# Performance work log

Measured on AMD Instinct MI355X. Metric: run time of the kernel, lower is better.

Reference implementation:

```python
import jax, jax.numpy as jnp
import numpy as np

N = 50000
E = 1600000
D = 128
BN_EPS = 1e-5


def setup_inputs() -> dict:
    key = jax.random.key(0)
    ks = jax.random.split(key, 6)
    feature = jax.random.normal(ks[0], (N, D), dtype=jnp.float32)
    snorm_n = jax.random.uniform(ks[1], (N, 1), dtype=jnp.float32)
    src = jax.random.randint(ks[2], (E,), 0, N, dtype=jnp.int64)
    dst = jax.random.randint(ks[3], (E,), 0, N, dtype=jnp.int64)
    W = jax.random.normal(ks[4], (D, D), dtype=jnp.float32) * (1.0 / np.sqrt(D))
    b = jax.random.normal(ks[5], (D,), dtype=jnp.float32) * 0.01
    gamma = jnp.ones((D,), dtype=jnp.float32)
    beta = jnp.zeros((D,), dtype=jnp.float32)
    return {"feature": feature, "snorm_n": snorm_n, "src": src, "dst": dst,
            "W": W, "b": b, "gamma": gamma, "beta": beta}


def reference(feature, snorm_n, src, dst, W, b, gamma, beta):
    # --- copy_src + mean reduce (DGL update_all) ---
    msg = feature[src]                                    # [E, D] gather
    agg = jax.ops.segment_sum(msg, dst, num_segments=N)   # [N, D] scatter-add
    deg = jax.ops.segment_sum(jnp.ones((src.shape[0],), feature.dtype), dst,
                              num_segments=N)             # [N]
    has_msg = deg > 0
    mean = agg / jnp.maximum(deg, 1.0)[:, None]
    # nodes with no incoming edges keep their original 'h' (DGL semantics)
    h = jnp.where(has_msg[:, None], mean, feature)
    # --- apply_nodes: linear ---
    h = h @ W.T + b
    # --- graph norm ---
    h = h * snorm_n
    # --- batch norm (training-mode stats, biased variance, eps=1e-5) ---
    mu = jnp.mean(h, axis=0)
    var = jnp.mean((h - mu) ** 2, axis=0)
    h = (h - mu) / jnp.sqrt(var + BN_EPS) * gamma + beta
    # --- activation + residual (dropout p=0 -> identity) ---
    h = jax.nn.relu(h)
    h = feature + h
    return h
```

## Files before the change

kernel.cpp:

```cpp
#include <hip/hip_runtime.h>

#define D 128
#define BN_EPS 1e-5f
#define ROWS 16
#define CHUNK 8192
#define CAP_SCAN 256
#define HSTRIDE 136
#define P2CAP 12288

typedef unsigned int u32;
typedef unsigned short u16;
typedef __attribute__((ext_vector_type(8))) __bf16 bf16x8;
typedef __attribute__((ext_vector_type(4))) float f32x4;

__device__ inline u32 pk_bf16(float x, float y) {
    u32 ux = __float_as_uint(x), uy = __float_as_uint(y);
    ux = (ux + 0x7fffu + ((ux >> 16) & 1u)) >> 16;
    uy = (uy + 0x7fffu + ((uy >> 16) & 1u)) >> 16;
    return ux | (uy << 16);
}

__global__ __launch_bounds__(256) void prep(const float* __restrict__ feat,
                                            u16* __restrict__ feat16,
                                            const float* __restrict__ W,
                                            u16* __restrict__ Wb,
                                            const int* __restrict__ dst,
                                            int* __restrict__ blkcnt,
                                            int ncast, int nch, int nedges) {
    __shared__ int cnt[256];
    const int b = blockIdx.x;
    if (b < ncast) {
        size_t i = ((size_t)b * 256 + threadIdx.x) * 8;
        float4 f0 = *reinterpret_cast<const float4*>(feat + i);
        float4 f1 = *reinterpret_cast<const float4*>(feat + i + 4);
        uint4 o;
        o.x = pk_bf16(f0.x, f0.y);
        o.y = pk_bf16(f0.z, f0.w);
        o.z = pk_bf16(f1.x, f1.y);
        o.w = pk_bf16(f1.z, f1.w);
        *reinterpret_cast<uint4*>(feat16 + i) = o;
    } else if (b < ncast + 8) {
        int t = (b - ncast) * 256 + threadIdx.x;
        int ct = t >> 8;
        int ks = (t >> 6) & 3;
        int l = t & 63;
        int row_w = 16 * ct + (l & 15);
        int col0 = ks * 32 + (l >> 4) * 8;
        float4 f0 = *reinterpret_cast<const float4*>(W + row_w * D + col0);
        float4 f1 = *reinterpret_cast<const float4*>(W + row_w * D + col0 + 4);
        uint4 o;
        o.x = pk_bf16(f0.x, f0.y);
        o.y = pk_bf16(f0.z, f0.w);
        o.z = pk_bf16(f1.x, f1.y);
        o.w = pk_bf16(f1.z, f1.w);
        *reinterpret_cast<uint4*>(Wb + (size_t)t * 8) = o;
    } else {
        const int c = b - ncast - 8;
        cnt[threadIdx.x] = 0;
        __syncthreads();
        const int e0 = c * CHUNK;
        for (int r = 0; r < CHUNK / 256; ++r) {
            int e = e0 + r * 256 + threadIdx.x;
            if (e < nedges) atomicAdd(&cnt[dst[e] >> 8], 1);
        }
        __syncthreads();
        blkcnt[(size_t)threadIdx.x * nch + c] = cnt[threadIdx.x];
    }
}

__global__ __launch_bounds__(CAP_SCAN) void scanB1(int* __restrict__ blkcnt,
                                                   int* __restrict__ gtot,
                                                   int nch) {
    __shared__ int s[CAP_SCAN];
    const int t = threadIdx.x;
    const size_t row = (size_t)blockIdx.x * nch;
    int v = (t < nch) ? blkcnt[row + t] : 0;
    s[t] = v;
    __syncthreads();
    for (int off = 1; off < CAP_SCAN; off <<= 1) {
        int u = (t >= off) ? s[t - off] : 0;
        __syncthreads();
        s[t] += u;
        __syncthreads();
    }
    if (t < nch) blkcnt[row + t] = s[t] - v;
    if (t == 0) gtot[blockIdx.x] = s[CAP_SCAN - 1];
}

__global__ __launch_bounds__(256) void scanB2(const int* __restrict__ gtot,
                                              int* __restrict__ bucket_base,
                                              int* __restrict__ bucket_cnt) {
    __shared__ int s[256];
    const int t = threadIdx.x;
    int v = gtot[t];
    s[t] = v;
    __syncthreads();
    for (int off = 1; off < 256; off <<= 1) {
        int u = (t >= off) ? s[t - off] : 0;
        __syncthreads();
        s[t] += u;
        __syncthreads();
    }
    bucket_base[t] = s[t] - v;
    bucket_cnt[t] = v;
}

__global__ __launch_bounds__(512) void passB(const int* __restrict__ src,
                                             const int* __restrict__ dst,
                                             const int* __restrict__ blkcnt,
                                             const int* __restrict__ bucket_base,
                                             u32* __restrict__ gpacked,
                                             int nch, int nedges) {
    __shared__ u32 sval[CHUNK];
    __shared__ u16 sbuck[CHUNK];
    __shared__ int cnt[256], lo[256], gbase[256];
    const int t = threadIdx.x;
    const int e0 = blockIdx.x * CHUNK;
    const int m = min(CHUNK, nedges - e0);
    if (t < 256) {
        cnt[t] = 0;
        gbase[t] = blkcnt[(size_t)t * nch + blockIdx.x] + bucket_base[t];
    }
    __syncthreads();
    for (int k = t; k < m; k += 512) atomicAdd(&cnt[dst[e0 + k] >> 8], 1);
    __syncthreads();
    int v = (t < 256) ? cnt[t] : 0;
    if (t < 256) lo[t] = v;
    __syncthreads();
    for (int off = 1; off < 256; off <<= 1) {
        int u = (t >= off && t < 256) ? lo[t - off] : 0;
        __syncthreads();
        if (t < 256) lo[t] += u;
        __syncthreads();
    }
    if (t < 256) { int ex = lo[t] - v; lo[t] = ex; cnt[t] = ex; }
    __syncthreads();
    for (int k = t; k < m; k += 512) {
        int d = dst[e0 + k];
        int b = d >> 8;
        int p = atomicAdd(&cnt[b], 1);
        sval[p] = (u32)src[e0 + k] | ((u32)(d & 255) << 16);
        sbuck[p] = (u16)b;
    }
    __syncthreads();
    for (int i = t; i < m; i += 512) {
        int b = sbuck[i];
        gpacked[gbase[b] + (i - lo[b])] = sval[i];
    }
}

__global__ __launch_bounds__(512) void pass2(const u32* __restrict__ gpacked,
                                             const int* __restrict__ bucket_base,
                                             const int* __restrict__ bucket_cnt,
                                             u16* __restrict__ epos,
                                             int* __restrict__ count,
                                             int* __restrict__ offs,
                                             int nnodes) {
    __shared__ u16 sepos[P2CAP];
    __shared__ int cnt[256], lo[256], cur[256];
    const int t = threadIdx.x;
    const int b = blockIdx.x;
    const int nE = bucket_cnt[b];
    const int base = bucket_base[b];
    if (t < 256) cnt[t] = 0;
    __syncthreads();
    for (int i = t; i < nE; i += 512) atomicAdd(&cnt[gpacked[base + i] >> 16], 1);
    __syncthreads();
    int v = (t < 256) ? cnt[t] : 0;
    if (t < 256) lo[t] = v;
    __syncthreads();
    for (int off = 1; off < 256; off <<= 1) {
        int u = (t >= off && t < 256) ? lo[t - off] : 0;
        __syncthreads();
        if (t < 256) lo[t] += u;
        __syncthreads();
    }
    if (t < 256) {
        int excl = lo[t] - v;
        int n = (b << 8) + t;
        if (n < nnodes) { count[n] = v; offs[n] = base + excl; }
        cur[t] = excl;
    }
    __syncthreads();
    if (nE <= P2CAP) {
        for (int i = t; i < nE; i += 512) {
            u32 p = gpacked[base + i];
            int pos = atomicAdd(&cur[p >> 16], 1);
            sepos[pos] = (u16)(p & 0xffffu);
        }
        __syncthreads();
        for (int i = t; i < nE; i += 512) epos[base + i] = sepos[i];
    } else {
        for (int i = t; i < nE; i += 512) {
            u32 p = gpacked[base + i];
            int pos = atomicAdd(&cur[p >> 16], 1);
            epos[base + pos] = (u16)(p & 0xffffu);
        }
    }
}

__global__ __launch_bounds__(256, 8) void fused_agg_linear(
        const float* __restrict__ feat,
        const u16* __restrict__ feat16,
        const float* __restrict__ snorm,
        const int* __restrict__ offs,
        const int* __restrict__ count,
        const u16* __restrict__ epos,
        const u16* __restrict__ Wb,
        const float* __restrict__ bias,
        float* __restrict__ y,
        float* __restrict__ partial) {
    __shared__ u16 hs16[ROWS][HSTRIDE];
    const int row0 = blockIdx.x * ROWS;
    const int wid = threadIdx.x >> 6;
    const int lane = threadIdx.x & 63;
    const int q = lane >> 4;
    const int ql = lane & 15;

#define LDB(s) (*reinterpret_cast<const uint4*>(feat16 + (size_t)(s) * D + 8 * ql))
#define ADD8(a, u) { \
    a[0] += __uint_as_float((u).x << 16); a[1] += __uint_as_float((u).x & 0xffff0000u); \
    a[2] += __uint_as_float((u).y << 16); a[3] += __uint_as_float((u).y & 0xffff0000u); \
    a[4] += __uint_as_float((u).z << 16); a[5] += __uint_as_float((u).z & 0xffff0000u); \
    a[6] += __uint_as_float((u).w << 16); a[7] += __uint_as_float((u).w & 0xffff0000u); }

    for (int rr = 0; rr < 4; ++rr) {
        const int r = wid * 4 + rr;
        const int n = row0 + r;
        const int dg = count[n];
        const u16* ep = epos + offs[n];
        float a0[8], a1[8];
        #pragma unroll
        for (int k = 0; k < 8; ++k) { a0[k] = 0.0f; a1[k] = 0.0f; }

        int j = 0;
        for (; j + 8 <= dg; j += 8) {
            int s0 = (int)ep[j + q];
            int s1 = (int)ep[j + 4 + q];
            uint4 u0 = LDB(s0);
            uint4 u1 = LDB(s1);
            ADD8(a0, u0);
            ADD8(a1, u1);
        }
        {
            int i0 = j + q, i1 = j + 4 + q;
            if (i0 < dg) { uint4 u0 = LDB((int)ep[i0]); ADD8(a0, u0); }
            if (i1 < dg) { uint4 u1 = LDB((int)ep[i1]); ADD8(a1, u1); }
        }

        float av[8];
        #pragma unroll
        for (int k = 0; k < 8; ++k) {
            float v = a0[k] + a1[k];
            v += __shfl_xor(v, 16, 64);
            v += __shfl_xor(v, 32, 64);
            av[k] = v;
        }
        if (dg > 0) {
            float inv = 1.0f / (float)dg;
            #pragma unroll
            for (int k = 0; k < 8; ++k) av[k] *= inv;
        } else {
            float4 f0 = *reinterpret_cast<const float4*>(feat + (size_t)n * D + 8 * ql);
            float4 f1 = *reinterpret_cast<const float4*>(feat + (size_t)n * D + 8 * ql + 4);
            av[0] = f0.x; av[1] = f0.y; av[2] = f0.z; av[3] = f0.w;
            av[4] = f1.x; av[5] = f1.y; av[6] = f1.z; av[7] = f1.w;
        }
        if (q == 0) {
            uint4 o4;
            o4.x = pk_bf16(av[0], av[1]);
            o4.y = pk_bf16(av[2], av[3]);
            o4.z = pk_bf16(av[4], av[5]);
            o4.w = pk_bf16(av[6], av[7]);
            *reinterpret_cast<uint4*>(&hs16[r][8 * ql]) = o4;
        }
    }
#undef LDB
#undef ADD8
    __syncthreads();

    bf16x8 afrag[4];
    const int arow = lane & 15;
    const int acol0 = (lane >> 4) * 8;
    #pragma unroll
    for (int ks = 0; ks < 4; ++ks)
        afrag[ks] = *reinterpret_cast<const bf16x8*>(&hs16[arow][ks * 32 + acol0]);

    #pragma unroll
    for (int c2 = 0; c2 < 2; ++c2) {
        const int ct = wid * 2 + c2;
        f32x4 acc = {0.f, 0.f, 0.f, 0.f};
        #pragma unroll
        for (int ks = 0; ks < 4; ++ks) {
            bf16x8 bfrag = *reinterpret_cast<const bf16x8*>(
                Wb + ((size_t)(ct * 4 + ks) * 64 + lane) * 8);
            acc = __builtin_amdgcn_mfma_f32_16x16x32_bf16(afrag[ks], bfrag, acc, 0, 0, 0);
        }
        const int col = ct * 16 + (lane & 15);
        const float bb = bias[col];
        float psum = 0.0f, psq = 0.0f;
        #pragma unroll
        for (int i = 0; i < 4; ++i) {
            const int rrow = (lane >> 4) * 4 + i;
            const int n = row0 + rrow;
            float v = (acc[i] + bb) * snorm[n];
            y[(size_t)n * D + col] = v;
            psum += v;
            psq += v * v;
        }
        psum += __shfl_xor(psum, 16, 64);
        psq  += __shfl_xor(psq, 16, 64);
        psum += __shfl_xor(psum, 32, 64);
        psq  += __shfl_xor(psq, 32, 64);
        if (lane < 16) {
            partial[(size_t)blockIdx.x * 256 + col] = psum;
            partial[(size_t)blockIdx.x * 256 + 128 + col] = psq;
        }
    }
}

__global__ __launch_bounds__(256) void bn_reduce(const float* __restrict__ partial,
                                                 const float* __restrict__ gamma,
                                                 const float* __restrict__ beta,
                                                 float* __restrict__ bnparam,
                                                 int nchunk, float inv_n) {
    const int d = blockIdx.x;
    float s = 0.0f, q = 0.0f;
    for (int b = threadIdx.x; b < nchunk; b += 256) {
        s += partial[(size_t)b * 256 + d];
        q += partial[(size_t)b * 256 + 128 + d];
    }
    for (int off = 32; off > 0; off >>= 1) {
        s += __shfl_down(s, off, 64);
        q += __shfl_down(q, off, 64);
    }
    __shared__ float ss[4], qq[4];
    int wid = threadIdx.x >> 6;
    int lane = threadIdx.x & 63;
    if (lane == 0) { ss[wid] = s; qq[wid] = q; }
    __syncthreads();
    if (threadIdx.x == 0) {
        float S = ss[0] + ss[1] + ss[2] + ss[3];
        float Q = qq[0] + qq[1] + qq[2] + qq[3];
        float mu = S * inv_n;
        float var = Q * inv_n - mu * mu;
        var = fmaxf(var, 0.0f);
        float rstd = rsqrtf(var + BN_EPS);
        float scale = gamma[d] * rstd;
        float shift = beta[d] - mu * scale;
        bnparam[d] = scale;
        bnparam[D + d] = shift;
    }
}

__global__ __launch_bounds__(256) void finalize(const float* __restrict__ feat,
                                                float* __restrict__ y,
                                                const float* __restrict__ bnparam,
                                                int total4) {
    int i = blockIdx.x * 256 + threadIdx.x;
    if (i >= total4) return;
    int c = i & 31;
    float4 v = reinterpret_cast<float4*>(y)[i];
    float4 f = reinterpret_cast<const float4*>(feat)[i];
    float4 sc = reinterpret_cast<const float4*>(bnparam)[c];
    float4 sh = reinterpret_cast<const float4*>(bnparam + D)[c];
    v.x = f.x + fmaxf(v.x * sc.x + sh.x, 0.0f);
    v.y = f.y + fmaxf(v.y * sc.y + sh.y, 0.0f);
    v.z = f.z + fmaxf(v.z * sc.z + sh.z, 0.0f);
    v.w = f.w + fmaxf(v.w * sc.w + sh.w, 0.0f);
    reinterpret_cast<float4*>(y)[i] = v;
}

extern "C" void kernel_launch(void* const* d_in, const int* in_sizes, int n_in,
                              void* d_out, int out_size, void* d_ws, size_t ws_size,
                              hipStream_t stream) {
    const float* feat  = (const float*)d_in[0];
    const float* snorm = (const float*)d_in[1];
    const int*   src   = (const int*)d_in[2];
    const int*   dst   = (const int*)d_in[3];
    const float* W     = (const float*)d_in[4];
    const float* bias  = (const float*)d_in[5];
    const float* gamma = (const float*)d_in[6];
    const float* beta  = (const float*)d_in[7];

    const int N = in_sizes[1];
    const int E = in_sizes[2];
    const int nblk = N / ROWS;
    const int nch = (E + CHUNK - 1) / CHUNK;
    const int nbuck = (N + 255) >> 8;
    const int ncast = (N * D) / (8 * 256);

    int* count       = (int*)d_ws;
    int* offs        = count + N;
    int* blkcnt      = offs + N;
    int* gtot        = blkcnt + (size_t)256 * nch;
    int* bucket_base = gtot + 256;
    int* bucket_cnt  = bucket_base + 256;
    u32* gpacked     = (u32*)(bucket_cnt + 256);
    u16* epos        = (u16*)(gpacked + E);
    u16* feat16      = epos + E;
    u16* Wb          = feat16 + (size_t)N * D;
    float* partial   = (float*)(Wb + D * D);
    float* bnparam   = partial + (size_t)nblk * 256;

    float* y = (float*)d_out;

    prep<<<ncast + 8 + nch, 256, 0, stream>>>(feat, feat16, W, Wb, dst,
                                              blkcnt, ncast, nch, E);

    scanB1<<<256, CAP_SCAN, 0, stream>>>(blkcnt, gtot, nch);
    scanB2<<<1, 256, 0, stream>>>(gtot, bucket_base, bucket_cnt);

    passB<<<nch, 512, 0, stream>>>(src, dst, blkcnt, bucket_base, gpacked, nch, E);

    pass2<<<nbuck, 512, 0, stream>>>(gpacked, bucket_base, bucket_cnt,
                                     epos, count, offs, N);

    fused_agg_linear<<<nblk, 256, 0, stream>>>(feat, feat16, snorm, offs, count,
                                               epos, Wb, bias, y, partial);

    bn_reduce<<<D, 256, 0, stream>>>(partial, gamma, beta, bnparam,
                                     nblk, 1.0f / (float)N);

    {
        int total4 = N * D / 4;
        finalize<<<(total4 + 255) / 256, 256, 0, stream>>>(feat, y, bnparam, total4);
    }
}
```

Before: 129.0 us.

## Unroll gather loop by 16 and split BN reduction into coalesced two-stage kernels

The neighbor-gather loop gains a 16-edge unrolled body, so each lane issues four independent bf16 row loads before accumulating, which increases memory-level parallelism for the latency-bound gather. The BN statistics reduction, previously 128 blocks each doing strided column reads over all partials, becomes two stages. In the first, 64 blocks each sum a contiguous slice of rows with coalesced 256-wide reads into a scratch buffer that reuses the blkcnt workspace. In the second, a single block finishes the sum and computes scale and shift. This adds one kernel launch and raises register pressure in the gather loop.

```diff
diff --git a/kernel.cpp b/kernel.cpp
--- a/kernel.cpp
+++ b/kernel.cpp
@@ -234,6 +234,20 @@
         for (int k = 0; k < 8; ++k) { a0[k] = 0.0f; a1[k] = 0.0f; }
 
         int j = 0;
+        for (; j + 16 <= dg; j += 16) {
+            int s0 = (int)ep[j + q];
+            int s1 = (int)ep[j + 4 + q];
+            int s2 = (int)ep[j + 8 + q];
+            int s3 = (int)ep[j + 12 + q];
+            uint4 u0 = LDB(s0);
+            uint4 u1 = LDB(s1);
+            uint4 u2 = LDB(s2);
+            uint4 u3 = LDB(s3);
+            ADD8(a0, u0);
+            ADD8(a1, u1);
+            ADD8(a0, u2);
+            ADD8(a1, u3);
+        }
         for (; j + 8 <= dg; j += 8) {
             int s0 = (int)ep[j + q];
             int s1 = (int)ep[j + 4 + q];
@@ -319,37 +333,35 @@
     }
 }
 
-__global__ __launch_bounds__(256) void bn_reduce(const float* __restrict__ partial,
-                                                 const float* __restrict__ gamma,
-                                                 const float* __restrict__ beta,
-                                                 float* __restrict__ bnparam,
-                                                 int nchunk, float inv_n) {
-    const int d = blockIdx.x;
-    float s = 0.0f, q = 0.0f;
-    for (int b = threadIdx.x; b < nchunk; b += 256) {
-        s += partial[(size_t)b * 256 + d];
-        q += partial[(size_t)b * 256 + 128 + d];
-    }
-    for (int off = 32; off > 0; off >>= 1) {
-        s += __shfl_down(s, off, 64);
-        q += __shfl_down(q, off, 64);
-    }
-    __shared__ float ss[4], qq[4];
-    int wid = threadIdx.x >> 6;
-    int lane = threadIdx.x & 63;
-    if (lane == 0) { ss[wid] = s; qq[wid] = q; }
-    __syncthreads();
-    if (threadIdx.x == 0) {
-        float S = ss[0] + ss[1] + ss[2] + ss[3];
-        float Q = qq[0] + qq[1] + qq[2] + qq[3];
+__global__ __launch_bounds__(256) void bn_r1(const float* __restrict__ partial,
+                                             float* __restrict__ pp, int nblk) {
+    const int rp = (nblk + 63) >> 6;
+    const int r0 = blockIdx.x * rp;
+    const int r1 = min(r0 + rp, nblk);
+    float s = 0.0f;
+    for (int r = r0; r < r1; ++r) s += partial[(size_t)r * 256 + threadIdx.x];
+    pp[blockIdx.x * 256 + threadIdx.x] = s;
+}
+
+__global__ __launch_bounds__(256) void bn_final(const float* __restrict__ pp,
+                                                const float* __restrict__ gamma,
+                                                const float* __restrict__ beta,
+                                                float* __restrict__ bnparam,
+                                                float inv_n) {
+    __shared__ float acc[256];
+    float s = 0.0f;
+    for (int g = 0; g < 64; ++g) s += pp[g * 256 + threadIdx.x];
+    acc[threadIdx.x] = s;
+    __syncthreads();
+    const int d = threadIdx.x;
+    if (d < 128) {
+        float S = acc[d], Q = acc[128 + d];
         float mu = S * inv_n;
-        float var = Q * inv_n - mu * mu;
-        var = fmaxf(var, 0.0f);
+        float var = fmaxf(Q * inv_n - mu * mu, 0.0f);
         float rstd = rsqrtf(var + BN_EPS);
         float scale = gamma[d] * rstd;
-        float shift = beta[d] - mu * scale;
         bnparam[d] = scale;
-        bnparam[D + d] = shift;
+        bnparam[D + d] = beta[d] - mu * scale;
     }
 }
 
@@ -402,6 +414,7 @@
     u16* Wb          = feat16 + (size_t)N * D;
     float* partial   = (float*)(Wb + D * D);
     float* bnparam   = partial + (size_t)nblk * 256;
+    float* pp        = (float*)blkcnt;
 
     float* y = (float*)d_out;
 
@@ -419,8 +432,8 @@
     fused_agg_linear<<<nblk, 256, 0, stream>>>(feat, feat16, snorm, offs, count,
                                                epos, Wb, bias, y, partial);
 
-    bn_reduce<<<D, 256, 0, stream>>>(partial, gamma, beta, bnparam,
-                                     nblk, 1.0f / (float)N);
+    bn_r1<<<64, 256, 0, stream>>>(partial, pp, nblk);
+    bn_final<<<1, 256, 0, stream>>>(pp, gamma, beta, bnparam, 1.0f / (float)N);
 
     {
         int total4 = N * D / 4;
```

Result: slower. 132.0 us, median of 2 (+2.3%).
